# Kernel tuning notes

Measured on AMD Instinct MI355X. Metric: run time of the kernel, lower is better.

## Reference

```python
import jax, jax.numpy as jnp
import numpy as np

N_NODES = 100000
N_EDGES = 1600000
IN_C, HID_C, OUT_C = 64, 64, 16


def _sage_conv(x, src, dst, W_l, b_l, W_r, num_nodes):
    # PyG SAGEConv (aggr='mean'): out = lin_l(mean_{j->i} x_j) + lin_r(x_i)
    # aggregate first (cheap small-d features), then one GEMM
    msg_sum = jax.ops.segment_sum(x[src], dst, num_segments=num_nodes)
    deg = jax.ops.segment_sum(jnp.ones_like(dst, dtype=x.dtype), dst,
                              num_segments=num_nodes)
    mean = msg_sum / jnp.maximum(deg, 1.0)[:, None]
    return mean @ W_l + b_l + x @ W_r


def setup_inputs() -> dict:
    key = jax.random.key(0)
    ks = jax.random.split(key, 8)
    x = jax.random.normal(ks[0], (N_NODES, IN_C), dtype=jnp.float32)
    edge_index = jax.random.randint(ks[1], (2, N_EDGES), 0, N_NODES, dtype=jnp.int64)
    # Glorot-ish init for weights; lin_l has bias, lin_r has none (PyG default)
    def glorot(k, fan_in, fan_out):
        s = jnp.sqrt(6.0 / (fan_in + fan_out))
        return jax.random.uniform(k, (fan_in, fan_out), jnp.float32, -s, s)
    return {
        "x": x,
        "edge_index": edge_index,
        "W1_l": glorot(ks[2], IN_C, HID_C),
        "b1": jnp.zeros((HID_C,), jnp.float32),
        "W1_r": glorot(ks[3], IN_C, HID_C),
        "W2_l": glorot(ks[4], HID_C, OUT_C),
        "b2": jnp.zeros((OUT_C,), jnp.float32),
        "W2_r": glorot(ks[5], HID_C, OUT_C),
    }


def reference(x, edge_index, W1_l, b1, W1_r, W2_l, b2, W2_r):
    src, dst = edge_index[0], edge_index[1]
    h = _sage_conv(x, src, dst, W1_l, b1, W1_r, N_NODES)
    h = jax.nn.relu(h)
    # dropout p=0.3 is identity in eval mode
    out = _sage_conv(h, src, dst, W2_l, b2, W2_r, N_NODES)
    return out
```

## Files before the change

kernel.cpp:

```cpp
#include <hip/hip_runtime.h>
#include <hip/hip_fp16.h>

#define N_NODES 100000
#define N_EDGES 1600000
#define IN_C 64
#define HID_C 64
#define OUT_C 16

#define BKT 256
#define BSH 8
#define NBKT 391
#define CAP 5120
#define GB 512
#define EPB 3125
#define NIT 13
#define G1B 1563

typedef _Float16 f16x8 __attribute__((ext_vector_type(8)));
typedef float f32x4 __attribute__((ext_vector_type(4)));
typedef float f32x16 __attribute__((ext_vector_type(16)));

__global__ __launch_bounds__(256) void k_merged1(
    const int* __restrict__ src, const int* __restrict__ dst,
    int* __restrict__ gcnt, int* __restrict__ binned,
    const float* __restrict__ x, const float* __restrict__ Wl,
    const float* __restrict__ Wr, const float* __restrict__ b,
    __half* __restrict__ p, __half* __restrict__ q) {
  __shared__ _Float16 sA[64 * 68];
  __shared__ _Float16 sW[128 * 68];
  int t = threadIdx.x;

  if (blockIdx.x < GB) {
    int* h   = (int*)sA;
    int* cur = (int*)sW;
    for (int i = t; i < NBKT; i += 256) h[i] = 0;
    __syncthreads();
    int base = blockIdx.x * EPB;
    int end = base + EPB;
    int dv[NIT], sv[NIT];
#pragma unroll
    for (int it = 0; it < NIT; ++it) {
      int e = base + t + it * 256;
      bool ok = (e < end);
      dv[it] = ok ? dst[e] : -1;
      sv[it] = ok ? src[e] : 0;
    }
#pragma unroll
    for (int it = 0; it < NIT; ++it)
      if (dv[it] >= 0) atomicAdd(&h[dv[it] >> BSH], 1);
    __syncthreads();
    for (int i = t; i < NBKT; i += 256) {
      int c = h[i];
      int b0 = (c > 0) ? atomicAdd(&gcnt[i], c) : 0;
      cur[i] = i * CAP + b0;
    }
    __syncthreads();
#pragma unroll
    for (int it = 0; it < NIT; ++it) {
      if (dv[it] >= 0) {
        int d = dv[it];
        int pos = atomicAdd(&cur[d >> BSH], 1);
        binned[pos] = (sv[it] << BSH) | (d & (BKT - 1));
      }
    }
    return;
  }

  int n0 = (blockIdx.x - GB) * 64;

  for (int f = t; f < 1024; f += 256) {
    int r = f >> 4, c4 = f & 15;
    int n = n0 + r;
    float4 v = {0.0f, 0.0f, 0.0f, 0.0f};
    if (n < N_NODES) v = *(const float4*)&x[(size_t)n * 64 + c4 * 4];
    union { _Float16 h[4]; float2 f2; } u;
    u.h[0] = (_Float16)v.x; u.h[1] = (_Float16)v.y;
    u.h[2] = (_Float16)v.z; u.h[3] = (_Float16)v.w;
    *(float2*)&sA[r * 68 + c4 * 4] = u.f2;
  }
  for (int f = t; f < 2048; f += 256) {
    int k = f >> 5, c4 = f & 31;
    float4 w = (c4 < 16) ? *(const float4*)&Wl[k * 64 + c4 * 4]
                         : *(const float4*)&Wr[k * 64 + (c4 - 16) * 4];
    int c = c4 * 4;
    sW[(c + 0) * 68 + k] = (_Float16)w.x;
    sW[(c + 1) * 68 + k] = (_Float16)w.y;
    sW[(c + 2) * 68 + k] = (_Float16)w.z;
    sW[(c + 3) * 68 + k] = (_Float16)w.w;
  }
  __syncthreads();

  int w = t >> 6, lane = t & 63;
  int m = lane & 31, half = lane >> 5;
  int rt = w & 1, cg = w >> 1;

  f32x16 acc[2];
#pragma unroll
  for (int r = 0; r < 16; ++r) { acc[0][r] = 0.0f; acc[1][r] = 0.0f; }

  const _Float16* pA = &sA[(rt * 32 + m) * 68 + half * 8];
  const _Float16* pB0 = &sW[(cg * 64 + m) * 68 + half * 8];
  const _Float16* pB1 = &sW[(cg * 64 + 32 + m) * 68 + half * 8];
#pragma unroll
  for (int kc = 0; kc < 4; ++kc) {
    union { f16x8 v; float2 f2[2]; } a, b0, b1;
    a.f2[0] = *(const float2*)(pA + kc * 16);
    a.f2[1] = *(const float2*)(pA + kc * 16 + 4);
    b0.f2[0] = *(const float2*)(pB0 + kc * 16);
    b0.f2[1] = *(const float2*)(pB0 + kc * 16 + 4);
    b1.f2[0] = *(const float2*)(pB1 + kc * 16);
    b1.f2[1] = *(const float2*)(pB1 + kc * 16 + 4);
    acc[0] = __builtin_amdgcn_mfma_f32_32x32x16_f16(a.v, b0.v, acc[0], 0, 0, 0);
    acc[1] = __builtin_amdgcn_mfma_f32_32x32x16_f16(a.v, b1.v, acc[1], 0, 0, 0);
  }

  if (cg == 0) {
#pragma unroll
    for (int tt = 0; tt < 2; ++tt) {
      int col = tt * 32 + m;
#pragma unroll
      for (int r = 0; r < 16; ++r) {
        int row = (r & 3) + 4 * half + 8 * (r >> 2);
        int n = n0 + rt * 32 + row;
        if (n < N_NODES) p[(size_t)n * 64 + col] = __float2half(acc[tt][r]);
      }
    }
  } else {
    float bias[2] = {b[m], b[32 + m]};
#pragma unroll
    for (int tt = 0; tt < 2; ++tt) {
      int col = tt * 32 + m;
#pragma unroll
      for (int r = 0; r < 16; ++r) {
        int row = (r & 3) + 4 * half + 8 * (r >> 2);
        int n = n0 + rt * 32 + row;
        if (n < N_NODES)
          q[(size_t)n * 64 + col] = __float2half(acc[tt][r] + bias[tt]);
      }
    }
  }
}

__global__ __launch_bounds__(1024) void k_fuse1c(
    const float4* __restrict__ p1, const int* __restrict__ gcnt,
    const int* __restrict__ binned, const float* __restrict__ W2l,
    const float* __restrict__ W2r, const float* __restrict__ b2,
    const float4* __restrict__ q1, int* __restrict__ csr,
    int* __restrict__ rowstart, int* __restrict__ cnt,
    __half* __restrict__ p2, float* __restrict__ q2) {
  __shared__ int hcnt[BKT];
  __shared__ int hscan[BKT];
  __shared__ int cur[BKT];
  __shared__ int lcsr[CAP];
  __shared__ _Float16 sH[256 * 68];
  __shared__ _Float16 sW[32 * 68];
  int b = blockIdx.x;
  int t = threadIdx.x;

  if (t < 512) {
    int k = t >> 3, c4v = t & 7;
    float4 w = (c4v < 4) ? *(const float4*)&W2l[k * 16 + c4v * 4]
                         : *(const float4*)&W2r[k * 16 + (c4v - 4) * 4];
    int c = c4v * 4;
    sW[(c + 0) * 68 + k] = (_Float16)w.x;
    sW[(c + 1) * 68 + k] = (_Float16)w.y;
    sW[(c + 2) * 68 + k] = (_Float16)w.z;
    sW[(c + 3) * 68 + k] = (_Float16)w.w;
  }
  if (t < BKT) hcnt[t] = 0;
  __syncthreads();

  int start = b * CAP;
  int total = gcnt[b];
  for (int i = t; i < total; i += 1024)
    atomicAdd(&hcnt[binned[start + i] & (BKT - 1)], 1);
  __syncthreads();
  int v = 0;
  if (t < BKT) {
    v = hcnt[t];
    hscan[t] = v;
  }
  __syncthreads();
  for (int st = 1; st < BKT; st <<= 1) {
    int a = 0;
    if (t < BKT && t >= st) a = hscan[t - st];
    __syncthreads();
    if (t < BKT) hscan[t] += a;
    __syncthreads();
  }
  if (t < BKT) {
    cur[t] = hscan[t] - v;
    int n = (b << BSH) + t;
    if (n < N_NODES) {
      rowstart[n] = start + hscan[t] - v;
      cnt[n] = v;
    }
  }
  __syncthreads();
  for (int i = t; i < total; i += 1024) {
    int vv = binned[start + i];
    int pos = atomicAdd(&cur[vv & (BKT - 1)], 1);
    lcsr[pos] = vv >> BSH;
  }
  __syncthreads();
  for (int i = t; i < total; i += 1024) csr[start + i] = lcsr[i];

  int g = t >> 3, c4 = t & 7;
  for (int r = g; r < BKT; r += 128) {
    int n = (b << BSH) + r;
    if (n < N_NODES) {
      int deg = hcnt[r];
      int row = hscan[r] - deg;
      float acc[8];
#pragma unroll
      for (int m = 0; m < 8; ++m) acc[m] = 0.0f;
      int j = 0;
      for (; j + 8 <= deg; j += 8) {
        int idx[8];
#pragma unroll
        for (int u = 0; u < 8; ++u) idx[u] = lcsr[row + j + u];
        float4 av[8];
#pragma unroll
        for (int u = 0; u < 8; ++u) av[u] = p1[idx[u] * 8 + c4];
#pragma unroll
        for (int u = 0; u < 8; ++u) {
          const __half2* h = (const __half2*)&av[u];
#pragma unroll
          for (int m = 0; m < 4; ++m) {
            float2 f = __half22float2(h[m]);
            acc[2 * m] += f.x;
            acc[2 * m + 1] += f.y;
          }
        }
      }
      for (; j < deg; ++j) {
        float4 a = p1[lcsr[row + j] * 8 + c4];
        const __half2* h = (const __half2*)&a;
#pragma unroll
        for (int m = 0; m < 4; ++m) {
          float2 f = __half22float2(h[m]);
          acc[2 * m] += f.x;
          acc[2 * m + 1] += f.y;
        }
      }
      float inv = 1.0f / fmaxf((float)deg, 1.0f);
      float4 qv = q1[n * 8 + c4];
      __half2* qh = (__half2*)&qv;
      union { __half2 h2[2]; float2 f2; } u01, u23;
#pragma unroll
      for (int m = 0; m < 2; ++m) {
        float2 f = __half22float2(qh[m]);
        float2 s;
        s.x = fmaxf(acc[2 * m] * inv + f.x, 0.0f);
        s.y = fmaxf(acc[2 * m + 1] * inv + f.y, 0.0f);
        u01.h2[m] = __float22half2_rn(s);
      }
#pragma unroll
      for (int m = 2; m < 4; ++m) {
        float2 f = __half22float2(qh[m]);
        float2 s;
        s.x = fmaxf(acc[2 * m] * inv + f.x, 0.0f);
        s.y = fmaxf(acc[2 * m + 1] * inv + f.y, 0.0f);
        u23.h2[m - 2] = __float22half2_rn(s);
      }
      *(float2*)&sH[r * 68 + c4 * 8] = u01.f2;
      *(float2*)&sH[r * 68 + c4 * 8 + 4] = u23.f2;
    } else {
      *(float2*)&sH[r * 68 + c4 * 8] = make_float2(0.0f, 0.0f);
      *(float2*)&sH[r * 68 + c4 * 8 + 4] = make_float2(0.0f, 0.0f);
    }
  }
  __syncthreads();

  int wv = t >> 6, lane = t & 63;
  int n16 = lane & 15, quad = lane >> 4;
  f32x4 aP, aQ;
#pragma unroll
  for (int r = 0; r < 4; ++r) { aP[r] = 0.0f; aQ[r] = 0.0f; }
  const _Float16* pA = &sH[(wv * 16 + n16) * 68 + quad * 8];
  const _Float16* pBP = &sW[n16 * 68 + quad * 8];
  const _Float16* pBQ = &sW[(16 + n16) * 68 + quad * 8];
#pragma unroll
  for (int kc = 0; kc < 2; ++kc) {
    union { f16x8 v; float2 f2[2]; } a, bp, bq;
    a.f2[0] = *(const float2*)(pA + kc * 32);
    a.f2[1] = *(const float2*)(pA + kc * 32 + 4);
    bp.f2[0] = *(const float2*)(pBP + kc * 32);
    bp.f2[1] = *(const float2*)(pBP + kc * 32 + 4);
    bq.f2[0] = *(const float2*)(pBQ + kc * 32);
    bq.f2[1] = *(const float2*)(pBQ + kc * 32 + 4);
    aP = __builtin_amdgcn_mfma_f32_16x16x32_f16(a.v, bp.v, aP, 0, 0, 0);
    aQ = __builtin_amdgcn_mfma_f32_16x16x32_f16(a.v, bq.v, aQ, 0, 0, 0);
  }
  float bias = b2[n16];
#pragma unroll
  for (int r = 0; r < 4; ++r) {
    int row = wv * 16 + quad * 4 + r;
    int n = (b << BSH) + row;
    if (n < N_NODES) {
      p2[(size_t)n * 16 + n16] = __float2half(aP[r]);
      q2[(size_t)n * 16 + n16] = aQ[r] + bias;
    }
  }
}

__global__ __launch_bounds__(256) void k_fuse2(
    const float4* __restrict__ p2, const float4* __restrict__ q2,
    const int* __restrict__ rowstart, const int* __restrict__ cnt,
    const int* __restrict__ csr, float4* __restrict__ out) {
  int t = threadIdx.x;
  int n = blockIdx.x * 128 + (t >> 1);
  if (n >= N_NODES) return;
  int c8 = t & 1;
  int row = rowstart[n];
  int deg = cnt[n];
  float acc[8];
#pragma unroll
  for (int m = 0; m < 8; ++m) acc[m] = 0.0f;
  int j = 0;
  for (; j + 8 <= deg; j += 8) {
    int idx[8];
#pragma unroll
    for (int u = 0; u < 8; ++u) idx[u] = csr[row + j + u];
    float4 av[8];
#pragma unroll
    for (int u = 0; u < 8; ++u) av[u] = p2[idx[u] * 2 + c8];
#pragma unroll
    for (int u = 0; u < 8; ++u) {
      const __half2* h = (const __half2*)&av[u];
#pragma unroll
      for (int m = 0; m < 4; ++m) {
        float2 f = __half22float2(h[m]);
        acc[2 * m] += f.x;
        acc[2 * m + 1] += f.y;
      }
    }
  }
  for (; j < deg; ++j) {
    float4 a = p2[csr[row + j] * 2 + c8];
    const __half2* h = (const __half2*)&a;
#pragma unroll
    for (int m = 0; m < 4; ++m) {
      float2 f = __half22float2(h[m]);
      acc[2 * m] += f.x;
      acc[2 * m + 1] += f.y;
    }
  }
  float inv = 1.0f / fmaxf((float)deg, 1.0f);
  float4 q0 = q2[n * 4 + c8 * 2];
  float4 q1v = q2[n * 4 + c8 * 2 + 1];
  float4 o0 = {acc[0] * inv + q0.x, acc[1] * inv + q0.y,
               acc[2] * inv + q0.z, acc[3] * inv + q0.w};
  float4 o1 = {acc[4] * inv + q1v.x, acc[5] * inv + q1v.y,
               acc[6] * inv + q1v.z, acc[7] * inv + q1v.w};
  out[n * 4 + c8 * 2] = o0;
  out[n * 4 + c8 * 2 + 1] = o1;
}

extern "C" void kernel_launch(void* const* d_in, const int* in_sizes, int n_in,
                              void* d_out, int out_size, void* d_ws, size_t ws_size,
                              hipStream_t stream) {
  const float* x   = (const float*)d_in[0];
  const int* edge  = (const int*)d_in[1];
  const int* src   = edge;
  const int* dst   = edge + N_EDGES;
  const float* W1l = (const float*)d_in[2];
  const float* b1  = (const float*)d_in[3];
  const float* W1r = (const float*)d_in[4];
  const float* W2l = (const float*)d_in[5];
  const float* b2  = (const float*)d_in[6];
  const float* W2r = (const float*)d_in[7];
  float* out = (float*)d_out;

  int* gcnt     = (int*)d_ws;
  int* rowstart = gcnt + 512;
  int* cnt      = rowstart + N_NODES;
  int* binned   = cnt + N_NODES;
  int* csr      = binned + NBKT * CAP;
  __half* p1    = (__half*)(csr + NBKT * CAP);
  __half* q1    = p1 + (size_t)N_NODES * 64;
  __half* p2    = q1 + (size_t)N_NODES * 64;
  float* q2     = (float*)(p2 + (size_t)N_NODES * 16);

  hipMemsetAsync(gcnt, 0, NBKT * sizeof(int), stream);

  k_merged1<<<GB + G1B, 256, 0, stream>>>(src, dst, gcnt, binned,
                                          x, W1l, W1r, b1, p1, q1);
  k_fuse1c<<<NBKT, 1024, 0, stream>>>((const float4*)p1, gcnt, binned,
                                      W2l, W2r, b2, (const float4*)q1,
                                      csr, rowstart, cnt, p2, q2);
  k_fuse2<<<(N_NODES + 127) / 128, 256, 0, stream>>>((const float4*)p2,
                                                     (const float4*)q2,
                                                     rowstart, cnt, csr,
                                                     (float4*)out);
}
```

Baseline: 186.6 us.

## Halve bucket size, pad global counters, and use wave-shuffle scan

Shrinks node buckets from 256 to 128 nodes, doubling the number of buckets so the CSR-building and layer-2 fused kernel launches 782 blocks of 512 threads instead of 391 blocks of 1024. This improves load spread across CUs and cuts LDS per block. Global bucket counters are padded to a 32-int stride to avoid atomic contention on shared cache lines. The shared-memory Hillis-Steele scan with many barriers is replaced by a single-wave shuffle scan. The risk is more global atomics in the binning phase and a tighter per-bucket capacity.

```diff
diff --git a/kernel.cpp b/kernel.cpp
--- a/kernel.cpp
+++ b/kernel.cpp
@@ -7,10 +7,11 @@
 #define HID_C 64
 #define OUT_C 16
 
-#define BKT 256
-#define BSH 8
-#define NBKT 391
-#define CAP 5120
+#define BKT 128
+#define BSH 7
+#define NBKT 782
+#define CAP 2816
+#define GSTR 32
 #define GB 512
 #define EPB 3125
 #define NIT 13
@@ -51,7 +52,7 @@
     __syncthreads();
     for (int i = t; i < NBKT; i += 256) {
       int c = h[i];
-      int b0 = (c > 0) ? atomicAdd(&gcnt[i], c) : 0;
+      int b0 = (c > 0) ? atomicAdd(&gcnt[i * GSTR], c) : 0;
       cur[i] = i * CAP + b0;
     }
     __syncthreads();
@@ -141,7 +142,7 @@
   }
 }
 
-__global__ __launch_bounds__(1024) void k_fuse1c(
+__global__ __launch_bounds__(512) void k_fuse1c(
     const float4* __restrict__ p1, const int* __restrict__ gcnt,
     const int* __restrict__ binned, const float* __restrict__ W2l,
     const float* __restrict__ W2r, const float* __restrict__ b2,
@@ -152,12 +153,12 @@
   __shared__ int hscan[BKT];
   __shared__ int cur[BKT];
   __shared__ int lcsr[CAP];
-  __shared__ _Float16 sH[256 * 68];
+  __shared__ _Float16 sH[BKT * 68];
   __shared__ _Float16 sW[32 * 68];
   int b = blockIdx.x;
   int t = threadIdx.x;
 
-  if (t < 512) {
+  {
     int k = t >> 3, c4v = t & 7;
     float4 w = (c4v < 4) ? *(const float4*)&W2l[k * 16 + c4v * 4]
                          : *(const float4*)&W2r[k * 16 + (c4v - 4) * 4];
@@ -171,42 +172,43 @@
   __syncthreads();
 
   int start = b * CAP;
-  int total = gcnt[b];
-  for (int i = t; i < total; i += 1024)
+  int total = gcnt[b * GSTR];
+  for (int i = t; i < total; i += 512)
     atomicAdd(&hcnt[binned[start + i] & (BKT - 1)], 1);
   __syncthreads();
-  int v = 0;
+  if (t < 64) {
+    int s0 = hcnt[t], s1 = hcnt[64 + t];
+    for (int st = 1; st < 64; st <<= 1) {
+      int a0 = __shfl_up(s0, st);
+      int a1 = __shfl_up(s1, st);
+      if (t >= st) { s0 += a0; s1 += a1; }
+    }
+    s1 += __shfl(s0, 63);
+    hscan[t] = s0;
+    hscan[64 + t] = s1;
+  }
+  __syncthreads();
   if (t < BKT) {
-    v = hcnt[t];
-    hscan[t] = v;
-  }
-  __syncthreads();
-  for (int st = 1; st < BKT; st <<= 1) {
-    int a = 0;
-    if (t < BKT && t >= st) a = hscan[t - st];
-    __syncthreads();
-    if (t < BKT) hscan[t] += a;
-    __syncthreads();
-  }
-  if (t < BKT) {
-    cur[t] = hscan[t] - v;
+    int v = hcnt[t];
+    int e0 = hscan[t] - v;
+    cur[t] = e0;
     int n = (b << BSH) + t;
     if (n < N_NODES) {
-      rowstart[n] = start + hscan[t] - v;
+      rowstart[n] = start + e0;
       cnt[n] = v;
     }
   }
   __syncthreads();
-  for (int i = t; i < total; i += 1024) {
+  for (int i = t; i < total; i += 512) {
     int vv = binned[start + i];
     int pos = atomicAdd(&cur[vv & (BKT - 1)], 1);
     lcsr[pos] = vv >> BSH;
   }
   __syncthreads();
-  for (int i = t; i < total; i += 1024) csr[start + i] = lcsr[i];
+  for (int i = t; i < total; i += 512) csr[start + i] = lcsr[i];
 
   int g = t >> 3, c4 = t & 7;
-  for (int r = g; r < BKT; r += 128) {
+  for (int r = g; r < BKT; r += 64) {
     int n = (b << BSH) + r;
     if (n < N_NODES) {
       int deg = hcnt[r];
@@ -373,7 +375,7 @@
   float* out = (float*)d_out;
 
   int* gcnt     = (int*)d_ws;
-  int* rowstart = gcnt + 512;
+  int* rowstart = gcnt + 25088;
   int* cnt      = rowstart + N_NODES;
   int* binned   = cnt + N_NODES;
   int* csr      = binned + NBKT * CAP;
@@ -382,13 +384,13 @@
   __half* p2    = q1 + (size_t)N_NODES * 64;
   float* q2     = (float*)(p2 + (size_t)N_NODES * 16);
 
-  hipMemsetAsync(gcnt, 0, NBKT * sizeof(int), stream);
+  hipMemsetAsync(gcnt, 0, NBKT * GSTR * sizeof(int), stream);
 
   k_merged1<<<GB + G1B, 256, 0, stream>>>(src, dst, gcnt, binned,
                                           x, W1l, W1r, b1, p1, q1);
-  k_fuse1c<<<NBKT, 1024, 0, stream>>>((const float4*)p1, gcnt, binned,
-                                      W2l, W2r, b2, (const float4*)q1,
-                                      csr, rowstart, cnt, p2, q2);
+  k_fuse1c<<<NBKT, 512, 0, stream>>>((const float4*)p1, gcnt, binned,
+                                     W2l, W2r, b2, (const float4*)q1,
+                                     csr, rowstart, cnt, p2, q2);
   k_fuse2<<<(N_NODES + 127) / 128, 256, 0, stream>>>((const float4*)p2,
                                                      (const float4*)q2,
                                                      rowstart, cnt, csr,
```

Result: slower. 191.5 us (+2.6%).

## Use fewer binning blocks and pad global bucket counters to separate cache lines

Applied to the files above, without the earlier changes.

The edge-binning phase now runs in 128 blocks of 12500 edges instead of 512 blocks of 3125, so about four times fewer global atomics land on the bucket counters. Each counter is spaced 32 ints apart so concurrent atomics hit different cache lines. The register-held edge arrays are replaced by a strided loop that reads dst twice, once per pass. The tradeoff is less parallelism in the binning phase, with each block running longer, and an extra global read of dst.

```diff
diff --git a/kernel.cpp b/kernel.cpp
--- a/kernel.cpp
+++ b/kernel.cpp
@@ -11,9 +11,9 @@
 #define BSH 8
 #define NBKT 391
 #define CAP 5120
-#define GB 512
-#define EPB 3125
-#define NIT 13
+#define GSTR 32
+#define GB 128
+#define EPB 12500
 #define G1B 1563
 
 typedef _Float16 f16x8 __attribute__((ext_vector_type(8)));
@@ -36,32 +36,20 @@
     for (int i = t; i < NBKT; i += 256) h[i] = 0;
     __syncthreads();
     int base = blockIdx.x * EPB;
-    int end = base + EPB;
-    int dv[NIT], sv[NIT];
-#pragma unroll
-    for (int it = 0; it < NIT; ++it) {
-      int e = base + t + it * 256;
-      bool ok = (e < end);
-      dv[it] = ok ? dst[e] : -1;
-      sv[it] = ok ? src[e] : 0;
-    }
-#pragma unroll
-    for (int it = 0; it < NIT; ++it)
-      if (dv[it] >= 0) atomicAdd(&h[dv[it] >> BSH], 1);
+    for (int i = t; i < EPB; i += 256)
+      atomicAdd(&h[dst[base + i] >> BSH], 1);
     __syncthreads();
     for (int i = t; i < NBKT; i += 256) {
       int c = h[i];
-      int b0 = (c > 0) ? atomicAdd(&gcnt[i], c) : 0;
+      int b0 = (c > 0) ? atomicAdd(&gcnt[i * GSTR], c) : 0;
       cur[i] = i * CAP + b0;
     }
     __syncthreads();
-#pragma unroll
-    for (int it = 0; it < NIT; ++it) {
-      if (dv[it] >= 0) {
-        int d = dv[it];
-        int pos = atomicAdd(&cur[d >> BSH], 1);
-        binned[pos] = (sv[it] << BSH) | (d & (BKT - 1));
-      }
+    for (int i = t; i < EPB; i += 256) {
+      int d = dst[base + i];
+      int s = src[base + i];
+      int pos = atomicAdd(&cur[d >> BSH], 1);
+      binned[pos] = (s << BSH) | (d & (BKT - 1));
     }
     return;
   }
@@ -171,7 +159,7 @@
   __syncthreads();
 
   int start = b * CAP;
-  int total = gcnt[b];
+  int total = gcnt[b * GSTR];
   for (int i = t; i < total; i += 1024)
     atomicAdd(&hcnt[binned[start + i] & (BKT - 1)], 1);
   __syncthreads();
@@ -373,7 +361,7 @@
   float* out = (float*)d_out;
 
   int* gcnt     = (int*)d_ws;
-  int* rowstart = gcnt + 512;
+  int* rowstart = gcnt + 12544;
   int* cnt      = rowstart + N_NODES;
   int* binned   = cnt + N_NODES;
   int* csr      = binned + NBKT * CAP;
@@ -382,7 +370,7 @@
   __half* p2    = q1 + (size_t)N_NODES * 64;
   float* q2     = (float*)(p2 + (size_t)N_NODES * 16);
 
-  hipMemsetAsync(gcnt, 0, NBKT * sizeof(int), stream);
+  hipMemsetAsync(gcnt, 0, NBKT * GSTR * sizeof(int), stream);
 
   k_merged1<<<GB + G1B, 256, 0, stream>>>(src, dst, gcnt, binned,
                                           x, W1l, W1r, b1, p1, q1);
```

Measured after the change: 182.0 us. 2.5% less time.
